# Optimization experiments

Measured on AMD Instinct MI355X. Metric: run time of the kernel, lower is better.

Reference implementation:

```python
import jax, jax.numpy as jnp
import numpy as np

N_NODES = 50000
N_EDGES = 500000
D_FEAT = 128
HIDDEN = 128
EPS = 1e-8


def _lin_init(key, fan_in, fan_out):
    return jax.random.normal(key, (fan_in, fan_out), dtype=jnp.float32) / np.sqrt(fan_in)


def setup_inputs() -> dict:
    key = jax.random.key(0)
    ks = jax.random.split(key, 16)
    h = jax.random.normal(ks[0], (N_NODES, D_FEAT), dtype=jnp.float32)
    coord = jax.random.normal(ks[1], (N_NODES, 3), dtype=jnp.float32)
    vel = jax.random.normal(ks[2], (N_NODES, 3), dtype=jnp.float32)
    edge_index = jax.random.randint(ks[3], (2, N_EDGES), 0, N_NODES, dtype=jnp.int32)
    return {
        "h": h, "coord": coord, "vel": vel, "edge_index": edge_index,
        "W_e1": _lin_init(ks[4], 2 * D_FEAT + 1, HIDDEN), "b_e1": jnp.zeros((HIDDEN,), jnp.float32),
        "W_e2": _lin_init(ks[5], HIDDEN, D_FEAT), "b_e2": jnp.zeros((D_FEAT,), jnp.float32),
        "W_c1": _lin_init(ks[6], D_FEAT, HIDDEN), "b_c1": jnp.zeros((HIDDEN,), jnp.float32),
        "W_c2": _lin_init(ks[7], HIDDEN, 1), "b_c2": jnp.zeros((1,), jnp.float32),
        "W_v1": _lin_init(ks[8], D_FEAT, HIDDEN), "b_v1": jnp.zeros((HIDDEN,), jnp.float32),
        "W_v2": _lin_init(ks[9], HIDDEN, 1), "b_v2": jnp.zeros((1,), jnp.float32),
        "W_n1": _lin_init(ks[10], 2 * D_FEAT, HIDDEN), "b_n1": jnp.zeros((HIDDEN,), jnp.float32),
        "W_n2": _lin_init(ks[11], HIDDEN, D_FEAT), "b_n2": jnp.zeros((D_FEAT,), jnp.float32),
    }


def reference(h, coord, vel, edge_index,
              W_e1, b_e1, W_e2, b_e2,
              W_c1, b_c1, W_c2, b_c2,
              W_v1, b_v1, W_v2, b_v2,
              W_n1, b_n1, W_n2, b_n2):
    act = jax.nn.silu
    r, c = edge_index[0], edge_index[1]
    n = coord.shape[0]

    # coord2radial with normalize=True
    diff = coord[r] - coord[c]                      # [E, 3]
    rad = jnp.sum(diff * diff, axis=-1, keepdims=True)  # [E, 1]
    norm = jnp.sqrt(jax.lax.stop_gradient(rad)) + EPS
    diff = diff / norm

    # edge_op: Linear -> act -> Linear -> act
    edge_in = jnp.concatenate([h[r], h[c], rad], axis=1)  # [E, 2D+1]
    m_ij = act(act(edge_in @ W_e1 + b_e1) @ W_e2 + b_e2)  # [E, D]

    # coord_op: Linear -> act -> Linear (scalar weight per edge)
    weights = act(m_ij @ W_c1 + b_c1) @ W_c2 + b_c2       # [E, 1]
    coors_sum = jax.ops.segment_sum(diff * weights, r, num_segments=n)  # [N, 3]

    # vel_op: Linear -> act -> Linear (scalar per node)
    vel_weights = act(h @ W_v1 + b_v1) @ W_v2 + b_v2      # [N, 1]
    coord_out = coord + coors_sum + vel * vel_weights

    # node aggregation + node_op: Linear -> act -> Linear
    m_i = jax.ops.segment_sum(m_ij, r, num_segments=h.shape[0])  # [N, D]
    agg = jnp.concatenate([h, m_i], axis=1)               # [N, 2D]
    h_out = act(agg @ W_n1 + b_n1) @ W_n2 + b_n2          # [N, D]
    return (h_out, coord_out)
```

## Files before the change

kernel.cpp:

```cpp
#include <hip/hip_runtime.h>
#include <stdint.h>

#define NN 50000
#define NE 500000
#define BLK 256
#define NEB ((NE + 127) / 128)
#define SST 136

#define BARRIER() asm volatile("s_waitcnt lgkmcnt(0)\n\ts_barrier" ::: "memory")

typedef __attribute__((ext_vector_type(8))) short bf16x8;
typedef __attribute__((ext_vector_type(4))) float f32x4;

__device__ __forceinline__ float silu(float x) {
    float e = __expf(-x);
    return x * __builtin_amdgcn_rcpf(1.0f + e);
}
__device__ __forceinline__ float bf2f(unsigned short s) {
    union { unsigned int u; float f; } v; v.u = ((unsigned int)s) << 16; return v.f;
}
__device__ __forceinline__ unsigned short f2bf(float f) {
    union { float f; unsigned int u; } v; v.f = f;
    return (unsigned short)((v.u + 0x7fffu + ((v.u >> 16) & 1u)) >> 16);
}
__device__ __forceinline__ unsigned int pack2(float a, float b) {
    unsigned int r;
    asm("v_cvt_pk_bf16_f32 %0, %1, %2" : "=v"(r) : "v"(a), "v"(b));
    return r;
}
__device__ __forceinline__ bf16x8 packf8(const float* p) {
    float4 f0 = *(const float4*)p; float4 f1 = *(const float4*)(p + 4);
    union { bf16x8 v; unsigned int u[4]; } o;
    o.u[0] = pack2(f0.x, f0.y); o.u[1] = pack2(f0.z, f0.w);
    o.u[2] = pack2(f1.x, f1.y); o.u[3] = pack2(f1.z, f1.w);
    return o.v;
}

__global__ void prep_h(const float* __restrict__ h, unsigned short* __restrict__ hb) {
    int i = blockIdx.x * 256 + threadIdx.x;
    if (i < NN * 128 / 4) {
        float4 v = ((const float4*)h)[i];
        uint2 o; o.x = pack2(v.x, v.y); o.y = pack2(v.z, v.w);
        ((uint2*)hb)[i] = o;
    }
}

__global__ void prep_w(const float* __restrict__ We1, const float* __restrict__ We2,
                       const float* __restrict__ Wc1, const float* __restrict__ Wv1,
                       const float* __restrict__ Wn1, const float* __restrict__ Wn2,
                       unsigned short* __restrict__ Wt1, unsigned short* __restrict__ Wt2,
                       unsigned short* __restrict__ Wt3, unsigned short* __restrict__ Wv1t,
                       unsigned short* __restrict__ Wn1t, unsigned short* __restrict__ Wn2t) {
    int i = blockIdx.x * 256 + threadIdx.x;
    if (i < 32768) {
        int j = i >> 8, k = i & 255;
        Wt1[i] = f2bf(We1[k * 128 + j]);
    } else if (i < 49152) {
        int t = i - 32768; int j = t >> 7, ks = t & 127;
        int k0 = (ks & 7) * 16 + (ks >> 3);
        Wt2[t] = f2bf(We2[k0 * 128 + j]);
    } else if (i < 65536) {
        int t = i - 49152; int j = t >> 7, ks = t & 127;
        int k0 = (ks & 7) * 16 + (ks >> 3);
        Wt3[t] = f2bf(Wc1[k0 * 128 + j]);
    } else if (i < 81920) {
        int t = i - 65536; int j = t >> 7, k = t & 127;
        Wv1t[t] = f2bf(Wv1[k * 128 + j]);
    } else if (i < 114688) {
        int t = i - 81920; int j = t >> 8, k = t & 255;
        int ksrc;
        if (k < 128) ksrc = k;
        else { int ks = k - 128; ksrc = 128 + (ks & 7) * 16 + (ks >> 3); }
// ... 15 lines not shown
    int t = threadIdx.x, idx = blockIdx.x * 256 + t;
    s[t] = (idx < NN) ? deg[idx] : 0;
    __syncthreads();
    for (int off = 128; off > 0; off >>= 1) {
        if (t < off) s[t] += s[t + off];
        __syncthreads();
    }
    if (t == 0) bsum[blockIdx.x] = s[0];
}

__global__ void scan_b(int* __restrict__ bsum) {
    __shared__ int s[256];
    int t = threadIdx.x;
    int v = (t < 196) ? bsum[t] : 0;
    s[t] = v;
    __syncthreads();
    for (int off = 1; off < 256; off <<= 1) {
        int x = (t >= off) ? s[t - off] : 0;
        __syncthreads();
        s[t] += x;
        __syncthreads();
    }
    if (t < 196) bsum[t] = s[t] - v;
}

__global__ void scan_c(const int* __restrict__ deg, const int* __restrict__ bsum,
                       int* __restrict__ rowptr) {
    __shared__ int s[256];
    int t = threadIdx.x, idx = blockIdx.x * 256 + t;
    int v = (idx < NN) ? deg[idx] : 0;
    s[t] = v;
    __syncthreads();
    for (int off = 1; off < 256; off <<= 1) {
        int x = (t >= off) ? s[t - off] : 0;
        __syncthreads();
        s[t] += x;
        __syncthreads();
    }
    if (idx < NN) rowptr[idx] = bsum[blockIdx.x] + s[t] - v;
    if (idx == 0) rowptr[NN] = NE;
}

__global__ void csr_fill(const int* __restrict__ eidx, const int* __restrict__ rowptr,
                         int* __restrict__ cursor,
                         int* __restrict__ csr_r, int* __restrict__ csr_c) {
    int e = blockIdx.x * 256 + threadIdx.x;
    if (e < NE) {
        int r = eidx[e], c = eidx[NE + e];
        int slot = rowptr[r] + atomicAdd(&cursor[r], 1);
        csr_r[slot] = r; csr_c[slot] = c;
    }
}

__device__ __forceinline__ void wpref256(const unsigned short* __restrict__ W, int halfk,
                                         uint4 w[8], int tid) {
#pragma unroll
    for (int t = 0; t < 8; ++t) {
        int idx = tid + t * 256; int j = idx >> 4, g = idx & 15;
        w[t] = *(const uint4*)(W + (size_t)j * 256 + halfk * 128 + g * 8);
    }
}
__device__ __forceinline__ void wpref128(const unsigned short* __restrict__ W,
                                         uint4 w[8], int tid) {
#pragma unroll
    for (int t = 0; t < 8; ++t) {
        int idx = tid + t * 256; int j = idx >> 4, g = idx & 15;
        w[t] = *(const uint4*)(W + (size_t)j * 128 + g * 8);
    }
}
__device__ __forceinline__ void wwrite(const uint4 w[8], unsigned short* sW, int tid) {
#pragma unroll
    for (int t = 0; t < 8; ++t) {
        int idx = tid + t * 256; int j = idx >> 4, g = idx & 15;
        *(uint4*)(sW + j * SST + g * 8) = w[t];
    }
}
__device__ __forceinline__ void mfma4(const bf16x8 a[2][4], const unsigned short* sW,
                                      int l16, int q, f32x4 acc[2][8]) {
#pragma unroll
    for (int kc = 0; kc < 4; ++kc)
#pragma unroll
        for (int ct = 0; ct < 8; ++ct) {
            bf16x8 b = *(const bf16x8*)(sW + (ct * 16 + l16) * SST + kc * 32 + q * 8);
            acc[0][ct] = __builtin_amdgcn_mfma_f32_16x16x32_bf16(a[0][kc], b, acc[0][ct], 0, 0, 0);
            acc[1][ct] = __builtin_amdgcn_mfma_f32_16x16x32_bf16(a[1][kc], b, acc[1][ct], 0, 0, 0);
        }
}

__global__ __launch_bounds__(BLK, 2) void egcl_edge(
    const float* __restrict__ coord,
    const int* __restrict__ csr_r, const int* __restrict__ csr_c,
    const unsigned short* __restrict__ hb,
    const unsigned short* __restrict__ Wt1,
    const unsigned short* __restrict__ Wt2,
    const unsigned short* __restrict__ Wt3,
    const float* __restrict__ We1,
    const float* __restrict__ be1, const float* __restrict__ be2,
    const float* __restrict__ bc1,
    const float* __restrict__ Wc2, const float* __restrict__ bc2,
    float* __restrict__ m_acc, float* __restrict__ c_sum)
{
    __shared__ __align__(16) unsigned short sAb[128 * SST];
    __shared__ __align__(16) unsigned short sW[128 * SST];
    __shared__ float sRad[128], sDif[128][3];
    __shared__ int sSeg[128];
    __shared__ float sBe1[128], sBe2[128], sBc1[128], sWlast[128], sWc2f[128];

    const int tid = threadIdx.x;
    const int wv = tid >> 6, lane = tid & 63, q = lane >> 4, l16 = lane & 15;
    const int e0 = blockIdx.x * 128;

    int nr[2], nc[2];
#pragma unroll
    for (int si = 0; si < 2; ++si) {
        int e = e0 + (wv * 2 + si) * 16 + l16;
        if (e >= NE) e = NE - 1;
        nr[si] = csr_r[e]; nc[si] = csr_c[e];
    }

    if (tid < 128) {
        sBe1[tid] = be1[tid]; sBe2[tid] = be2[tid]; sBc1[tid] = bc1[tid];
        sWlast[tid] = We1[256 * 128 + tid]; sWc2f[tid] = Wc2[tid];
        int s = e0 + tid; int sc = (s < NE) ? s : (NE - 1);
        int r = csr_r[sc], c = csr_c[sc];
        sSeg[tid] = (s < NE) ? r : -1;
        float dx = coord[r * 3 + 0] - coord[c * 3 + 0];
        float dy = coord[r * 3 + 1] - coord[c * 3 + 1];
        float dz = coord[r * 3 + 2] - coord[c * 3 + 2];
        float rad = fmaf(dx, dx, fmaf(dy, dy, dz * dz));
        float inv = 1.0f / (sqrtf(rad) + 1e-8f);
        sRad[tid] = rad;
        sDif[tid][0] = dx * inv; sDif[tid][1] = dy * inv; sDif[tid][2] = dz * inv;
    }

    uint4 wA[8], wB[8];
    wpref256(Wt1, 0, wA, tid);
    wpref256(Wt1, 1, wB, tid);
    bf16x8 ar[2][4], ac[2][4];
#pragma unroll
    for (int si = 0; si < 2; ++si)
#pragma unroll
        for (int kc = 0; kc < 4; ++kc) {
            ar[si][kc] = *(const bf16x8*)(hb + (size_t)nr[si] * 128 + kc * 32 + q * 8);
            ac[si][kc] = *(const bf16x8*)(hb + (size_t)nc[si] * 128 + kc * 32 + q * 8);
        }
    wwrite(wA, sW, tid);
    wwrite(wB, sAb, tid);
    wpref128(Wt2, wA, tid);
    const float bc2v = bc2[0];
    BARRIER();

    f32x4 acc[2][8];
#pragma unroll
    for (int si = 0; si < 2; ++si)
#pragma unroll
        for (int ct = 0; ct < 8; ++ct) acc[si][ct] = (f32x4){0.f, 0.f, 0.f, 0.f};

    mfma4(ar, sW, l16, q, acc);
    mfma4(ac, sAb, l16, q, acc);
    BARRIER();
    wwrite(wA, sW, tid);
    wpref128(Wt3, wA, tid);

#pragma unroll
    for (int si = 0; si < 2; ++si)
#pragma unroll
        for (int r = 0; r < 4; ++r) {
            int row = (wv * 2 + si) * 16 + q * 4 + r;
            float rad = sRad[row];
            float v[8];
#pragma unroll
            for (int ct = 0; ct < 8; ++ct) {
                int col = ct * 16 + l16;
                v[ct] = silu(acc[si][ct][r] + rad * sWlast[col] + sBe1[col]);
            }
            uint4 pk = make_uint4(pack2(v[0], v[1]), pack2(v[2], v[3]),
                                  pack2(v[4], v[5]), pack2(v[6], v[7]));
            *(uint4*)(sAb + row * SST + l16 * 8) = pk;
        }
    BARRIER();

#pragma unroll
    for (int si = 0; si < 2; ++si)
#pragma unroll
        for (int ct = 0; ct < 8; ++ct) acc[si][ct] = (f32x4){0.f, 0.f, 0.f, 0.f};
    {
        bf16x8 a[2][4];
#pragma unroll
        for (int si = 0; si < 2; ++si) {
            int row = (wv * 2 + si) * 16 + l16;
#pragma unroll
            for (int kc = 0; kc < 4; ++kc)
                a[si][kc] = *(const bf16x8*)(sAb + row * SST + kc * 32 + q * 8);
        }
        mfma4(a, sW, l16, q, acc);
    }
#pragma unroll
    for (int si = 0; si < 2; ++si)
#pragma unroll
        for (int r = 0; r < 4; ++r) {
            float v[8];
#pragma unroll
            for (int ct = 0; ct < 8; ++ct) v[ct] = silu(acc[si][ct][r] + sBe2[ct * 16 + l16]);
            int row = (wv * 2 + si) * 16 + q * 4 + r;
            *(uint4*)(sAb + row * SST + l16 * 8) =
                make_uint4(pack2(v[0], v[1]), pack2(v[2], v[3]),
                           pack2(v[4], v[5]), pack2(v[6], v[7]));
        }
    BARRIER();
    wwrite(wA, sW, tid);
    BARRIER();

#pragma unroll
    for (int si = 0; si < 2; ++si)
#pragma unroll
        for (int ct = 0; ct < 8; ++ct) acc[si][ct] = (f32x4){0.f, 0.f, 0.f, 0.f};
    {
        bf16x8 a[2][4];
#pragma unroll
        for (int si = 0; si < 2; ++si) {
            int row = (wv * 2 + si) * 16 + l16;
#pragma unroll
            for (int kc = 0; kc < 4; ++kc)
                a[si][kc] = *(const bf16x8*)(sAb + row * SST + kc * 32 + q * 8);
        }
        mfma4(a, sW, l16, q, acc);
    }
#pragma unroll
    for (int si = 0; si < 2; ++si) {
        float p[4];
#pragma unroll
        for (int r = 0; r < 4; ++r) {
            float s = 0.f;
#pragma unroll
            for (int ct = 0; ct < 8; ++ct) {
                int col = ct * 16 + l16;
                float t = silu(acc[si][ct][r] + sBc1[col]);
                s = fmaf(t, sWc2f[col], s);
            }
            p[r] = s;
        }
#pragma unroll
        for (int m = 1; m < 16; m <<= 1)
#pragma unroll
            for (int r = 0; r < 4; ++r) p[r] += __shfl_xor(p[r], m, 16);
        if (l16 == 0) {
#pragma unroll
            for (int r = 0; r < 4; ++r) {
                int row = (wv * 2 + si) * 16 + q * 4 + r;
                int rn = sSeg[row];
                if (rn >= 0) {
                    float wgt = p[r] + bc2v;
                    atomicAdd(&c_sum[(size_t)rn * 3 + 0], sDif[row][0] * wgt);
                    atomicAdd(&c_sum[(size_t)rn * 3 + 1], sDif[row][1] * wgt);
                    atomicAdd(&c_sum[(size_t)rn * 3 + 2], sDif[row][2] * wgt);
                }
            }
        }
    }

    {
        int p = tid & 127, half = tid >> 7;
        int base = half * 64;
        float run = 0.f;
        int cur = sSeg[base];
        bool openL = true;
#pragma unroll 1
        for (int i0 = 0; i0 < 64; i0 += 4) {
            float v[4]; int rr[4];
#pragma unroll
            for (int j = 0; j < 4; ++j) {
                int row = base + i0 + j;
                rr[j] = sSeg[row];
                v[j] = bf2f(sAb[row * SST + p]);
            }
#pragma unroll
            for (int j = 0; j < 4; ++j) {
                if (rr[j] != cur) {
                    if (cur >= 0) {
                        float* dst = &m_acc[(size_t)cur * 128 + p];
                        if (openL) atomicAdd(dst, run);
                        else       *dst = run;
                    }
                    run = 0.f; cur = rr[j]; openL = false;
                }
                run += v[j];
            }
        }
        if (cur >= 0) atomicAdd(&m_acc[(size_t)cur * 128 + p], run);
    }
}

__global__ __launch_bounds__(BLK, 3) void egcl_node(
    const unsigned short* __restrict__ hb,
    const float* __restrict__ coord,
    const float* __restrict__ vel,
    const unsigned short* __restrict__ Wv1t, const float* __restrict__ bv1,
    const float* __restrict__ Wv2, const float* __restrict__ bv2,
    const unsigned short* __restrict__ Wn1t, const float* __restrict__ bn1,
    const unsigned short* __restrict__ Wn2t, const float* __restrict__ bn2,
    const float* __restrict__ m_acc, const float* __restrict__ c_sum,
    float* __restrict__ out_h, float* __restrict__ out_c)
{
    __shared__ __align__(16) unsigned short sAb[128 * SST];
    __shared__ float sBv1[128], sWv2f[128], sBn1[128], sBn2[128];

    const int tid = threadIdx.x;
    const int wv = tid >> 6, lane = tid & 63, q = lane >> 4, l16 = lane & 15;
    const int n0 = blockIdx.x * 128;
    int nval = NN - n0; if (nval > 128) nval = 128;

    if (tid < 128) {
        sBv1[tid] = bv1[tid]; sWv2f[tid] = Wv2[tid];
        sBn1[tid] = bn1[tid]; sBn2[tid] = bn2[tid];
    }
    const float bv2v = bv2[0];

    bf16x8 ah[2][4], am[2][4];
#pragma unroll
    for (int si = 0; si < 2; ++si) {
        int row = (wv * 2 + si) * 16 + l16;
        int nn = n0 + row; if (nn >= NN) nn = NN - 1;
#pragma unroll
        for (int kc = 0; kc < 4; ++kc) {
            ah[si][kc] = *(const bf16x8*)(hb + (size_t)nn * 128 + kc * 32 + q * 8);
            am[si][kc] = packf8(m_acc + (size_t)nn * 128 + kc * 32 + q * 8);
        }
    }

    BARRIER();

    f32x4 acc[2][8];
#pragma unroll
    for (int si = 0; si < 2; ++si)
#pragma unroll
        for (int ct = 0; ct < 8; ++ct) acc[si][ct] = (f32x4){0.f, 0.f, 0.f, 0.f};
#pragma unroll
    for (int kc = 0; kc < 4; ++kc)
#pragma unroll
        for (int ct = 0; ct < 8; ++ct) {
            bf16x8 b = *(const bf16x8*)(Wv1t + (size_t)(ct * 16 + l16) * 128 + kc * 32 + q * 8);
            acc[0][ct] = __builtin_amdgcn_mfma_f32_16x16x32_bf16(ah[0][kc], b, acc[0][ct], 0, 0, 0);
            acc[1][ct] = __builtin_amdgcn_mfma_f32_16x16x32_bf16(ah[1][kc], b, acc[1][ct], 0, 0, 0);
        }
#pragma unroll
    for (int si = 0; si < 2; ++si) {
// ... 86 lines not shown
    for (int si = 0; si < 2; ++si)
#pragma unroll
        for (int r = 0; r < 4; ++r) {
            int row = (wv * 2 + si) * 16 + q * 4 + r;
            if (row < nval) {
                float* orow = out_h + (size_t)(n0 + row) * 128;
#pragma unroll
                for (int ct = 0; ct < 8; ++ct)
                    orow[ct * 16 + l16] = acc[si][ct][r] + sBn2[ct * 16 + l16];
            }
        }
}

extern "C" void kernel_launch(void* const* d_in, const int* in_sizes, int n_in,
                              void* d_out, int out_size, void* d_ws, size_t ws_size,
                              hipStream_t stream) {
    const float* h     = (const float*)d_in[0];
    const float* coord = (const float*)d_in[1];
    const float* vel   = (const float*)d_in[2];
    const int*   eidx  = (const int*)d_in[3];
    const float* We1 = (const float*)d_in[4];
    const float* be1 = (const float*)d_in[5];
    const float* We2 = (const float*)d_in[6];
    const float* be2 = (const float*)d_in[7];
    const float* Wc1 = (const float*)d_in[8];
    const float* bc1 = (const float*)d_in[9];
    const float* Wc2 = (const float*)d_in[10];
    const float* bc2 = (const float*)d_in[11];
    const float* Wv1 = (const float*)d_in[12];
    const float* bv1 = (const float*)d_in[13];
    const float* Wv2 = (const float*)d_in[14];
    const float* bv2 = (const float*)d_in[15];
    const float* Wn1 = (const float*)d_in[16];
    const float* bn1 = (const float*)d_in[17];
    const float* Wn2 = (const float*)d_in[18];
    const float* bn2 = (const float*)d_in[19];

    char* ws = (char*)d_ws;
    float* m_acc = (float*)ws;
    float* c_sum = (float*)(ws + 25600000);
    unsigned short* hb   = (unsigned short*)(ws + 26200064);
    unsigned short* Wt1  = (unsigned short*)(ws + 39000064);
    unsigned short* Wt2  = (unsigned short*)(ws + 39065600);
    unsigned short* Wt3  = (unsigned short*)(ws + 39098368);
    unsigned short* Wv1t = (unsigned short*)(ws + 39131136);
    unsigned short* Wn1t = (unsigned short*)(ws + 39163904);
    unsigned short* Wn2t = (unsigned short*)(ws + 39229440);
    int* deg    = (int*)(ws + 39262208);
    int* cursor = (int*)(ws + 39462208);
    int* rowptr = (int*)(ws + 39662208);
    int* bsum   = (int*)(ws + 39862272);
    int* csr_r  = (int*)(ws + 39863296);
    int* csr_c  = (int*)(ws + 41863296);

    hipMemsetAsync(ws, 0, 26200000, stream);
    hipMemsetAsync(ws + 39262208, 0, 400000, stream);

    prep_h<<<6250, 256, 0, stream>>>(h, hb);
    prep_w<<<512, 256, 0, stream>>>(We1, We2, Wc1, Wv1, Wn1, Wn2,
                                    Wt1, Wt2, Wt3, Wv1t, Wn1t, Wn2t);

    csr_count<<<1954, 256, 0, stream>>>(eidx, deg);
    scan_a<<<196, 256, 0, stream>>>(deg, bsum);
    scan_b<<<1, 256, 0, stream>>>(bsum);
    scan_c<<<196, 256, 0, stream>>>(deg, bsum, rowptr);
    csr_fill<<<1954, 256, 0, stream>>>(eidx, rowptr, cursor, csr_r, csr_c);

    egcl_edge<<<NEB, BLK, 0, stream>>>(
        coord, csr_r, csr_c, hb, Wt1, Wt2, Wt3,
        We1, be1, be2, bc1, Wc2, bc2, m_acc, c_sum);

    float* out_h = (float*)d_out;
    float* out_c = out_h + (size_t)NN * 128;
    egcl_node<<<(NN + 127) / 128, BLK, 0, stream>>>(
        hb, coord, vel, Wv1t, bv1, Wv2, bv2, Wn1t, bn1, Wn2t, bn2,
        m_acc, c_sum, out_h, out_c);
}
```

Measured before the change: 393.6 us.

## Split edge-kernel work across 8 waves with one 16-row tile each

```diff
diff --git a/kernel.cpp b/kernel.cpp
--- a/kernel.cpp
+++ b/kernel.cpp
@@ -3,7 +3,7 @@
 
 #define NN 50000
 #define NE 500000
-#define BLK 256
+#define EBLK 512
 #define NEB ((NE + 127) / 128)
 #define SST 136
 
@@ -140,41 +140,40 @@
 }
 
 __device__ __forceinline__ void wpref256(const unsigned short* __restrict__ W, int halfk,
-                                         uint4 w[8], int tid) {
-#pragma unroll
-    for (int t = 0; t < 8; ++t) {
-        int idx = tid + t * 256; int j = idx >> 4, g = idx & 15;
+                                         uint4 w[4], int tid) {
+#pragma unroll
+    for (int t = 0; t < 4; ++t) {
+        int idx = tid + t * 512; int j = idx >> 4, g = idx & 15;
         w[t] = *(const uint4*)(W + (size_t)j * 256 + halfk * 128 + g * 8);
     }
 }
 __device__ __forceinline__ void wpref128(const unsigned short* __restrict__ W,
-                                         uint4 w[8], int tid) {
-#pragma unroll
-    for (int t = 0; t < 8; ++t) {
-        int idx = tid + t * 256; int j = idx >> 4, g = idx & 15;
+                                         uint4 w[4], int tid) {
+#pragma unroll
+    for (int t = 0; t < 4; ++t) {
+        int idx = tid + t * 512; int j = idx >> 4, g = idx & 15;
         w[t] = *(const uint4*)(W + (size_t)j * 128 + g * 8);
     }
 }
-__device__ __forceinline__ void wwrite(const uint4 w[8], unsigned short* sW, int tid) {
-#pragma unroll
-    for (int t = 0; t < 8; ++t) {
-        int idx = tid + t * 256; int j = idx >> 4, g = idx & 15;
+__device__ __forceinline__ void wwrite(const uint4 w[4], unsigned short* sW, int tid) {
+#pragma unroll
+    for (int t = 0; t < 4; ++t) {
+        int idx = tid + t * 512; int j = idx >> 4, g = idx & 15;
         *(uint4*)(sW + j * SST + g * 8) = w[t];
     }
 }
-__device__ __forceinline__ void mfma4(const bf16x8 a[2][4], const unsigned short* sW,
-                                      int l16, int q, f32x4 acc[2][8]) {
+__device__ __forceinline__ void mfma4(const bf16x8 a[4], const unsigned short* sW,
+                                      int l16, int q, f32x4 acc[8]) {
 #pragma unroll
     for (int kc = 0; kc < 4; ++kc)
 #pragma unroll
         for (int ct = 0; ct < 8; ++ct) {
             bf16x8 b = *(const bf16x8*)(sW + (ct * 16 + l16) * SST + kc * 32 + q * 8);
-            acc[0][ct] = __builtin_amdgcn_mfma_f32_16x16x32_bf16(a[0][kc], b, acc[0][ct], 0, 0, 0);
-            acc[1][ct] = __builtin_amdgcn_mfma_f32_16x16x32_bf16(a[1][kc], b, acc[1][ct], 0, 0, 0);
-        }
-}
-
-__global__ __launch_bounds__(BLK, 2) void egcl_edge(
+            acc[ct] = __builtin_amdgcn_mfma_f32_16x16x32_bf16(a[kc], b, acc[ct], 0, 0, 0);
+        }
+}
+
+__global__ __launch_bounds__(EBLK, 4) void egcl_edge(
     const float* __restrict__ coord,
     const int* __restrict__ csr_r, const int* __restrict__ csr_c,
     const unsigned short* __restrict__ hb,
@@ -197,13 +196,9 @@
     const int wv = tid >> 6, lane = tid & 63, q = lane >> 4, l16 = lane & 15;
     const int e0 = blockIdx.x * 128;
 
-    int nr[2], nc[2];
-#pragma unroll
-    for (int si = 0; si < 2; ++si) {
-        int e = e0 + (wv * 2 + si) * 16 + l16;
-        if (e >= NE) e = NE - 1;
-        nr[si] = csr_r[e]; nc[si] = csr_c[e];
-    }
+    int er = e0 + wv * 16 + l16;
+    if (er >= NE) er = NE - 1;
+    const int nr = csr_r[er], nc = csr_c[er];
 
     if (tid < 128) {
         sBe1[tid] = be1[tid]; sBe2[tid] = be2[tid]; sBc1[tid] = bc1[tid];
@@ -220,28 +215,24 @@
         sDif[tid][0] = dx * inv; sDif[tid][1] = dy * inv; sDif[tid][2] = dz * inv;
     }
 
-    uint4 wA[8], wB[8];
+    uint4 wA[4], wB[4];
     wpref256(Wt1, 0, wA, tid);
     wpref256(Wt1, 1, wB, tid);
-    bf16x8 ar[2][4], ac[2][4];
-#pragma unroll
-    for (int si = 0; si < 2; ++si)
-#pragma unroll
-        for (int kc = 0; kc < 4; ++kc) {
-            ar[si][kc] = *(const bf16x8*)(hb + (size_t)nr[si] * 128 + kc * 32 + q * 8);
-            ac[si][kc] = *(const bf16x8*)(hb + (size_t)nc[si] * 128 + kc * 32 + q * 8);
-        }
+    bf16x8 ar[4], ac[4];
+#pragma unroll
+    for (int kc = 0; kc < 4; ++kc) {
+        ar[kc] = *(const bf16x8*)(hb + (size_t)nr * 128 + kc * 32 + q * 8);
+        ac[kc] = *(const bf16x8*)(hb + (size_t)nc * 128 + kc * 32 + q * 8);
+    }
     wwrite(wA, sW, tid);
     wwrite(wB, sAb, tid);
     wpref128(Wt2, wA, tid);
     const float bc2v = bc2[0];
     BARRIER();
 
-    f32x4 acc[2][8];
-#pragma unroll
-    for (int si = 0; si < 2; ++si)
-#pragma unroll
-        for (int ct = 0; ct < 8; ++ct) acc[si][ct] = (f32x4){0.f, 0.f, 0.f, 0.f};
+    f32x4 acc[8];
+#pragma unroll
+    for (int ct = 0; ct < 8; ++ct) acc[ct] = (f32x4){0.f, 0.f, 0.f, 0.f};
 
     mfma4(ar, sW, l16, q, acc);
     mfma4(ac, sAb, l16, q, acc);
@@ -250,79 +241,64 @@
     wpref128(Wt3, wA, tid);
 
 #pragma unroll
-    for (int si = 0; si < 2; ++si)
+    for (int r = 0; r < 4; ++r) {
+        int row = wv * 16 + q * 4 + r;
+        float rad = sRad[row];
+        float v[8];
+#pragma unroll
+        for (int ct = 0; ct < 8; ++ct) {
+            int col = ct * 16 + l16;
+            v[ct] = silu(acc[ct][r] + rad * sWlast[col] + sBe1[col]);
+        }
+        uint4 pk = make_uint4(pack2(v[0], v[1]), pack2(v[2], v[3]),
+                              pack2(v[4], v[5]), pack2(v[6], v[7]));
+        *(uint4*)(sAb + row * SST + l16 * 8) = pk;
+    }
+    BARRIER();
+
+#pragma unroll
+    for (int ct = 0; ct < 8; ++ct) acc[ct] = (f32x4){0.f, 0.f, 0.f, 0.f};
+    {
+        bf16x8 a[4];
+        int row = wv * 16 + l16;
+#pragma unroll
+        for (int kc = 0; kc < 4; ++kc)
+            a[kc] = *(const bf16x8*)(sAb + row * SST + kc * 32 + q * 8);
+        mfma4(a, sW, l16, q, acc);
+    }
+#pragma unroll
+    for (int r = 0; r < 4; ++r) {
+        float v[8];
+#pragma unroll
+        for (int ct = 0; ct < 8; ++ct) v[ct] = silu(acc[ct][r] + sBe2[ct * 16 + l16]);
+        int row = wv * 16 + q * 4 + r;
+        *(uint4*)(sAb + row * SST + l16 * 8) =
+            make_uint4(pack2(v[0], v[1]), pack2(v[2], v[3]),
+                       pack2(v[4], v[5]), pack2(v[6], v[7]));
+    }
+    BARRIER();
+    wwrite(wA, sW, tid);
+    BARRIER();
+
+#pragma unroll
+    for (int ct = 0; ct < 8; ++ct) acc[ct] = (f32x4){0.f, 0.f, 0.f, 0.f};
+    {
+        bf16x8 a[4];
+        int row = wv * 16 + l16;
+#pragma unroll
+        for (int kc = 0; kc < 4; ++kc)
+            a[kc] = *(const bf16x8*)(sAb + row * SST + kc * 32 + q * 8);
+        mfma4(a, sW, l16, q, acc);
+    }
+    {
+        float p[4];
 #pragma unroll
         for (int r = 0; r < 4; ++r) {
-            int row = (wv * 2 + si) * 16 + q * 4 + r;
-            float rad = sRad[row];
-            float v[8];
+            float s = 0.f;
 #pragma unroll
             for (int ct = 0; ct < 8; ++ct) {
                 int col = ct * 16 + l16;
-                v[ct] = silu(acc[si][ct][r] + rad * sWlast[col] + sBe1[col]);
-            }
-            uint4 pk = make_uint4(pack2(v[0], v[1]), pack2(v[2], v[3]),
-                                  pack2(v[4], v[5]), pack2(v[6], v[7]));
-            *(uint4*)(sAb + row * SST + l16 * 8) = pk;
-        }
-    BARRIER();
-
-#pragma unroll
-    for (int si = 0; si < 2; ++si)
-#pragma unroll
-        for (int ct = 0; ct < 8; ++ct) acc[si][ct] = (f32x4){0.f, 0.f, 0.f, 0.f};
-    {
-        bf16x8 a[2][4];
-#pragma unroll
-        for (int si = 0; si < 2; ++si) {
-            int row = (wv * 2 + si) * 16 + l16;
-#pragma unroll
-            for (int kc = 0; kc < 4; ++kc)
-                a[si][kc] = *(const bf16x8*)(sAb + row * SST + kc * 32 + q * 8);
-        }
-        mfma4(a, sW, l16, q, acc);
-    }
-#pragma unroll
-    for (int si = 0; si < 2; ++si)
-#pragma unroll
-        for (int r = 0; r < 4; ++r) {
-            float v[8];
-#pragma unroll
-            for (int ct = 0; ct < 8; ++ct) v[ct] = silu(acc[si][ct][r] + sBe2[ct * 16 + l16]);
-            int row = (wv * 2 + si) * 16 + q * 4 + r;
-            *(uint4*)(sAb + row * SST + l16 * 8) =
-                make_uint4(pack2(v[0], v[1]), pack2(v[2], v[3]),
-                           pack2(v[4], v[5]), pack2(v[6], v[7]));
-        }
-    BARRIER();
-    wwrite(wA, sW, tid);
-    BARRIER();
-
-#pragma unroll
-    for (int si = 0; si < 2; ++si)
-#pragma unroll
-        for (int ct = 0; ct < 8; ++ct) acc[si][ct] = (f32x4){0.f, 0.f, 0.f, 0.f};
-    {
-        bf16x8 a[2][4];
-#pragma unroll
-        for (int si = 0; si < 2; ++si) {
-            int row = (wv * 2 + si) * 16 + l16;
-#pragma unroll
-            for (int kc = 0; kc < 4; ++kc)
-                a[si][kc] = *(const bf16x8*)(sAb + row * SST + kc * 32 + q * 8);
-        }
-        mfma4(a, sW, l16, q, acc);
-    }
-#pragma unroll
-    for (int si = 0; si < 2; ++si) {
-        float p[4];
-#pragma unroll
-        for (int r = 0; r < 4; ++r) {
-            float s = 0.f;
-#pragma unroll
-            for (int ct = 0; ct < 8; ++ct) {
-                int col = ct * 16 + l16;
-                float t = silu(acc[si][ct][r] + sBc1[col]);
+                float t = silu(acc[ct][r] + sBc1[col]);
                 s = fmaf(t, sWc2f[col], s);
             }
             p[r] = s;
@@ -334,7 +310,7 @@
         if (l16 == 0) {
 #pragma unroll
             for (int r = 0; r < 4; ++r) {
-                int row = (wv * 2 + si) * 16 + q * 4 + r;
+                int row = wv * 16 + q * 4 + r;
                 int rn = sSeg[row];
                 if (rn >= 0) {
                     float wgt = p[r] + bc2v;
@@ -347,13 +323,13 @@
     }
 
     {
-        int p = tid & 127, half = tid >> 7;
-        int base = half * 64;
+        int p = tid & 127, qtr = tid >> 7;
+        int base = qtr * 32;
         float run = 0.f;
         int cur = sSeg[base];
         bool openL = true;
 #pragma unroll 1
-        for (int i0 = 0; i0 < 64; i0 += 4) {
+        for (int i0 = 0; i0 < 32; i0 += 4) {
             float v[4]; int rr[4];
 #pragma unroll
             for (int j = 0; j < 4; ++j) {
@@ -378,7 +354,7 @@
     }
 }
 
-__global__ __launch_bounds__(BLK, 3) void egcl_node(
+__global__ __launch_bounds__(256, 3) void egcl_node(
     const unsigned short* __restrict__ hb,
     const float* __restrict__ coord,
     const float* __restrict__ vel,
@@ -585,13 +561,13 @@
     scan_c<<<196, 256, 0, stream>>>(deg, bsum, rowptr);
     csr_fill<<<1954, 256, 0, stream>>>(eidx, rowptr, cursor, csr_r, csr_c);
 
-    egcl_edge<<<NEB, BLK, 0, stream>>>(
+    egcl_edge<<<NEB, EBLK, 0, stream>>>(
         coord, csr_r, csr_c, hb, Wt1, Wt2, Wt3,
         We1, be1, be2, bc1, Wc2, bc2, m_acc, c_sum);
 
     float* out_h = (float*)d_out;
     float* out_c = out_h + (size_t)NN * 128;
-    egcl_node<<<(NN + 127) / 128, BLK, 0, stream>>>(
+    egcl_node<<<(NN + 127) / 128, 256, 0, stream>>>(
         hb, coord, vel, Wv1t, bv1, Wv2, bv2, Wn1t, bn1, Wn2t, bn2,
         m_acc, c_sum, out_h, out_c);
 }
```

After: 394.3 us. About the same (+0.2%).

## Split edge-MLP columns across 8 waves with 512-thread edge blocks

Applied to the files above, without the earlier changes.

```diff
diff --git a/kernel.cpp b/kernel.cpp
--- a/kernel.cpp
+++ b/kernel.cpp
@@ -3,7 +3,7 @@
 
 #define NN 50000
 #define NE 500000
-#define BLK 256
+#define EBLK 512
 #define NEB ((NE + 127) / 128)
 #define SST 136
 
@@ -140,41 +140,42 @@
 }
 
 __device__ __forceinline__ void wpref256(const unsigned short* __restrict__ W, int halfk,
-                                         uint4 w[8], int tid) {
-#pragma unroll
-    for (int t = 0; t < 8; ++t) {
-        int idx = tid + t * 256; int j = idx >> 4, g = idx & 15;
+                                         uint4 w[4], int tid) {
+#pragma unroll
+    for (int t = 0; t < 4; ++t) {
+        int idx = tid + t * 512; int j = idx >> 4, g = idx & 15;
         w[t] = *(const uint4*)(W + (size_t)j * 256 + halfk * 128 + g * 8);
     }
 }
 __device__ __forceinline__ void wpref128(const unsigned short* __restrict__ W,
-                                         uint4 w[8], int tid) {
-#pragma unroll
-    for (int t = 0; t < 8; ++t) {
-        int idx = tid + t * 256; int j = idx >> 4, g = idx & 15;
+                                         uint4 w[4], int tid) {
+#pragma unroll
+    for (int t = 0; t < 4; ++t) {
+        int idx = tid + t * 512; int j = idx >> 4, g = idx & 15;
         w[t] = *(const uint4*)(W + (size_t)j * 128 + g * 8);
     }
 }
-__device__ __forceinline__ void wwrite(const uint4 w[8], unsigned short* sW, int tid) {
-#pragma unroll
-    for (int t = 0; t < 8; ++t) {
-        int idx = tid + t * 256; int j = idx >> 4, g = idx & 15;
+__device__ __forceinline__ void wwrite(const uint4 w[4], unsigned short* sW, int tid) {
+#pragma unroll
+    for (int t = 0; t < 4; ++t) {
+        int idx = tid + t * 512; int j = idx >> 4, g = idx & 15;
         *(uint4*)(sW + j * SST + g * 8) = w[t];
     }
 }
-__device__ __forceinline__ void mfma4(const bf16x8 a[2][4], const unsigned short* sW,
-                                      int l16, int q, f32x4 acc[2][8]) {
+__device__ __forceinline__ void mfma_h(const bf16x8 a[2][4], const unsigned short* sB,
+                                       int l16, int q, int ch, f32x4 acc[2][4]) {
 #pragma unroll
     for (int kc = 0; kc < 4; ++kc)
 #pragma unroll
-        for (int ct = 0; ct < 8; ++ct) {
-            bf16x8 b = *(const bf16x8*)(sW + (ct * 16 + l16) * SST + kc * 32 + q * 8);
-            acc[0][ct] = __builtin_amdgcn_mfma_f32_16x16x32_bf16(a[0][kc], b, acc[0][ct], 0, 0, 0);
-            acc[1][ct] = __builtin_amdgcn_mfma_f32_16x16x32_bf16(a[1][kc], b, acc[1][ct], 0, 0, 0);
-        }
-}
-
-__global__ __launch_bounds__(BLK, 2) void egcl_edge(
+        for (int c = 0; c < 4; ++c) {
+            int g = ch * 4 + c;
+            bf16x8 b = *(const bf16x8*)(sB + (g * 16 + l16) * SST + kc * 32 + q * 8);
+            acc[0][c] = __builtin_amdgcn_mfma_f32_16x16x32_bf16(a[0][kc], b, acc[0][c], 0, 0, 0);
+            acc[1][c] = __builtin_amdgcn_mfma_f32_16x16x32_bf16(a[1][kc], b, acc[1][c], 0, 0, 0);
+        }
+}
+
+__global__ __launch_bounds__(EBLK, 4) void egcl_edge(
     const float* __restrict__ coord,
     const int* __restrict__ csr_r, const int* __restrict__ csr_c,
     const unsigned short* __restrict__ hb,
@@ -195,12 +196,14 @@
 
     const int tid = threadIdx.x;
     const int wv = tid >> 6, lane = tid & 63, q = lane >> 4, l16 = lane & 15;
+    const int wq = wv & 3, ch = wv >> 2;
+    const int rb = wq * 32;
     const int e0 = blockIdx.x * 128;
 
     int nr[2], nc[2];
 #pragma unroll
     for (int si = 0; si < 2; ++si) {
-        int e = e0 + (wv * 2 + si) * 16 + l16;
+        int e = e0 + rb + si * 16 + l16;
         if (e >= NE) e = NE - 1;
         nr[si] = csr_r[e]; nc[si] = csr_c[e];
     }
@@ -220,7 +223,7 @@
         sDif[tid][0] = dx * inv; sDif[tid][1] = dy * inv; sDif[tid][2] = dz * inv;
     }
 
-    uint4 wA[8], wB[8];
+    uint4 wA[4], wB[4];
     wpref256(Wt1, 0, wA, tid);
     wpref256(Wt1, 1, wB, tid);
     bf16x8 ar[2][4], ac[2][4];
@@ -237,14 +240,14 @@
     const float bc2v = bc2[0];
     BARRIER();
 
-    f32x4 acc[2][8];
-#pragma unroll
-    for (int si = 0; si < 2; ++si)
-#pragma unroll
-        for (int ct = 0; ct < 8; ++ct) acc[si][ct] = (f32x4){0.f, 0.f, 0.f, 0.f};
-
-    mfma4(ar, sW, l16, q, acc);
-    mfma4(ac, sAb, l16, q, acc);
+    f32x4 acc[2][4];
+#pragma unroll
+    for (int si = 0; si < 2; ++si)
+#pragma unroll
+        for (int c = 0; c < 4; ++c) acc[si][c] = (f32x4){0.f, 0.f, 0.f, 0.f};
+
+    mfma_h(ar, sW, l16, q, ch, acc);
+    mfma_h(ac, sAb, l16, q, ch, acc);
     BARRIER();
     wwrite(wA, sW, tid);
     wpref128(Wt3, wA, tid);
@@ -253,65 +256,70 @@
     for (int si = 0; si < 2; ++si)
 #pragma unroll
         for (int r = 0; r < 4; ++r) {
-            int row = (wv * 2 + si) * 16 + q * 4 + r;
+            int row = rb + si * 16 + q * 4 + r;
             float rad = sRad[row];
-            float v[8];
-#pragma unroll
-            for (int ct = 0; ct < 8; ++ct) {
-                int col = ct * 16 + l16;
-                v[ct] = silu(acc[si][ct][r] + rad * sWlast[col] + sBe1[col]);
-            }
-            uint4 pk = make_uint4(pack2(v[0], v[1]), pack2(v[2], v[3]),
-                                  pack2(v[4], v[5]), pack2(v[6], v[7]));
-            *(uint4*)(sAb + row * SST + l16 * 8) = pk;
+            float v[4];
+#pragma unroll
+            for (int c = 0; c < 4; ++c) {
+                int col = (ch * 4 + c) * 16 + l16;
+                v[c] = silu(acc[si][c][r] + rad * sWlast[col] + sBe1[col]);
+            }
+            *(uint2*)(sAb + row * SST + l16 * 8 + ch * 4) =
+                make_uint2(pack2(v[0], v[1]), pack2(v[2], v[3]));
         }
     BARRIER();
 
 #pragma unroll
     for (int si = 0; si < 2; ++si)
 #pragma unroll
-        for (int ct = 0; ct < 8; ++ct) acc[si][ct] = (f32x4){0.f, 0.f, 0.f, 0.f};
+        for (int c = 0; c < 4; ++c) acc[si][c] = (f32x4){0.f, 0.f, 0.f, 0.f};
     {
         bf16x8 a[2][4];
 #pragma unroll
         for (int si = 0; si < 2; ++si) {
-            int row = (wv * 2 + si) * 16 + l16;
+            int row = rb + si * 16 + l16;
 #pragma unroll
             for (int kc = 0; kc < 4; ++kc)
                 a[si][kc] = *(const bf16x8*)(sAb + row * SST + kc * 32 + q * 8);
         }
-        mfma4(a, sW, l16, q, acc);
-    }
+        mfma_h(a, sW, l16, q, ch, acc);
+    }
+    uint2 mu[2][4];
 #pragma unroll
     for (int si = 0; si < 2; ++si)
 #pragma unroll
         for (int r = 0; r < 4; ++r) {
-            float v[8];
-#pragma unroll
-            for (int ct = 0; ct < 8; ++ct) v[ct] = silu(acc[si][ct][r] + sBe2[ct * 16 + l16]);
-            int row = (wv * 2 + si) * 16 + q * 4 + r;
-            *(uint4*)(sAb + row * SST + l16 * 8) =
-                make_uint4(pack2(v[0], v[1]), pack2(v[2], v[3]),
-                           pack2(v[4], v[5]), pack2(v[6], v[7]));
+            float v[4];
+#pragma unroll
+            for (int c = 0; c < 4; ++c)
+                v[c] = silu(acc[si][c][r] + sBe2[(ch * 4 + c) * 16 + l16]);
+            mu[si][r] = make_uint2(pack2(v[0], v[1]), pack2(v[2], v[3]));
         }
     BARRIER();
+#pragma unroll
+    for (int si = 0; si < 2; ++si)
+#pragma unroll
+        for (int r = 0; r < 4; ++r) {
+            int row = rb + si * 16 + q * 4 + r;
+            *(uint2*)(sAb + row * SST + l16 * 8 + ch * 4) = mu[si][r];
+        }
     wwrite(wA, sW, tid);
     BARRIER();
 
 #pragma unroll
     for (int si = 0; si < 2; ++si)
 #pragma unroll
-        for (int ct = 0; ct < 8; ++ct) acc[si][ct] = (f32x4){0.f, 0.f, 0.f, 0.f};
+        for (int c = 0; c < 4; ++c) acc[si][c] = (f32x4){0.f, 0.f, 0.f, 0.f};
     {
         bf16x8 a[2][4];
 #pragma unroll
         for (int si = 0; si < 2; ++si) {
-            int row = (wv * 2 + si) * 16 + l16;
+            int row = rb + si * 16 + l16;
 #pragma unroll
             for (int kc = 0; kc < 4; ++kc)
                 a[si][kc] = *(const bf16x8*)(sAb + row * SST + kc * 32 + q * 8);
         }
-        mfma4(a, sW, l16, q, acc);
+        mfma_h(a, sW, l16, q, ch, acc);
     }
 #pragma unroll
     for (int si = 0; si < 2; ++si) {
@@ -320,9 +328,9 @@
         for (int r = 0; r < 4; ++r) {
             float s = 0.f;
 #pragma unroll
-            for (int ct = 0; ct < 8; ++ct) {
-                int col = ct * 16 + l16;
-                float t = silu(acc[si][ct][r] + sBc1[col]);
+            for (int c = 0; c < 4; ++c) {
+                int col = (ch * 4 + c) * 16 + l16;
+                float t = silu(acc[si][c][r] + sBc1[col]);
                 s = fmaf(t, sWc2f[col], s);
             }
             p[r] = s;
@@ -334,10 +342,10 @@
         if (l16 == 0) {
 #pragma unroll
             for (int r = 0; r < 4; ++r) {
-                int row = (wv * 2 + si) * 16 + q * 4 + r;
+                int row = rb + si * 16 + q * 4 + r;
                 int rn = sSeg[row];
                 if (rn >= 0) {
-                    float wgt = p[r] + bc2v;
+                    float wgt = p[r] + (ch == 0 ? bc2v : 0.0f);
                     atomicAdd(&c_sum[(size_t)rn * 3 + 0], sDif[row][0] * wgt);
                     atomicAdd(&c_sum[(size_t)rn * 3 + 1], sDif[row][1] * wgt);
                     atomicAdd(&c_sum[(size_t)rn * 3 + 2], sDif[row][2] * wgt);
@@ -347,13 +355,13 @@
     }
 
     {
-        int p = tid & 127, half = tid >> 7;
-        int base = half * 64;
+        int p = tid & 127, qtr = tid >> 7;
+        int base = qtr * 32;
         float run = 0.f;
         int cur = sSeg[base];
         bool openL = true;
 #pragma unroll 1
-        for (int i0 = 0; i0 < 64; i0 += 4) {
+        for (int i0 = 0; i0 < 32; i0 += 4) {
             float v[4]; int rr[4];
 #pragma unroll
             for (int j = 0; j < 4; ++j) {
@@ -378,7 +386,7 @@
     }
 }
 
-__global__ __launch_bounds__(BLK, 3) void egcl_node(
+__global__ __launch_bounds__(256, 3) void egcl_node(
     const unsigned short* __restrict__ hb,
     const float* __restrict__ coord,
     const float* __restrict__ vel,
@@ -585,13 +593,13 @@
     scan_c<<<196, 256, 0, stream>>>(deg, bsum, rowptr);
     csr_fill<<<1954, 256, 0, stream>>>(eidx, rowptr, cursor, csr_r, csr_c);
 
-    egcl_edge<<<NEB, BLK, 0, stream>>>(
+    egcl_edge<<<NEB, EBLK, 0, stream>>>(
         coord, csr_r, csr_c, hb, Wt1, Wt2, Wt3,
         We1, be1, be2, bc1, Wc2, bc2, m_acc, c_sum);
 
     float* out_h = (float*)d_out;
     float* out_c = out_h + (size_t)NN * 128;
-    egcl_node<<<(NN + 127) / 128, BLK, 0, stream>>>(
+    egcl_node<<<(NN + 127) / 128, 256, 0, stream>>>(
         hb, coord, vel, Wv1t, bv1, Wv2, bv2, Wn1t, bn1, Wn2t, bn2,
         m_acc, c_sum, out_h, out_c);
 }
```

New measurement: 447.4 us. +13.7%, slower.

## Precompute per-node first-layer projections and gather them instead of raw features

Applied to the files above, without the earlier changes.

```diff
diff --git a/kernel.cpp b/kernel.cpp
--- a/kernel.cpp
+++ b/kernel.cpp
@@ -3,11 +3,11 @@
 
 #define NN 50000
 #define NE 500000
-#define BLK 256
 #define NEB ((NE + 127) / 128)
 #define SST 136
 
 #define BARRIER() asm volatile("s_waitcnt lgkmcnt(0)\n\ts_barrier" ::: "memory")
+#define WAVE_SYNC() asm volatile("s_waitcnt lgkmcnt(0)" ::: "memory")
 
 typedef __attribute__((ext_vector_type(8))) short bf16x8;
 typedef __attribute__((ext_vector_type(4))) float f32x4;
@@ -18,6 +18,12 @@
 }
 __device__ __forceinline__ float bf2f(unsigned short s) {
     union { unsigned int u; float f; } v; v.u = ((unsigned int)s) << 16; return v.f;
+}
+__device__ __forceinline__ float bflo(unsigned int u) {
+    union { unsigned int u; float f; } v; v.u = u << 16; return v.f;
+}
+__device__ __forceinline__ float bfhi(unsigned int u) {
+    union { unsigned int u; float f; } v; v.u = u & 0xffff0000u; return v.f;
 }
 __device__ __forceinline__ unsigned short f2bf(float f) {
     union { float f; unsigned int u; } v; v.f = f;
@@ -139,27 +145,20 @@
     }
 }
 
-__device__ __forceinline__ void wpref256(const unsigned short* __restrict__ W, int halfk,
-                                         uint4 w[8], int tid) {
+__device__ __forceinline__ void stage256(const unsigned short* __restrict__ W, int halfk,
+                                         unsigned short* sW, int tid) {
 #pragma unroll
     for (int t = 0; t < 8; ++t) {
         int idx = tid + t * 256; int j = idx >> 4, g = idx & 15;
-        w[t] = *(const uint4*)(W + (size_t)j * 256 + halfk * 128 + g * 8);
-    }
-}
-__device__ __forceinline__ void wpref128(const unsigned short* __restrict__ W,
-                                         uint4 w[8], int tid) {
+        *(uint4*)(sW + j * SST + g * 8) = *(const uint4*)(W + (size_t)j * 256 + halfk * 128 + g * 8);
+    }
+}
+__device__ __forceinline__ void stage128(const unsigned short* __restrict__ W,
+                                         unsigned short* sW, int tid) {
 #pragma unroll
     for (int t = 0; t < 8; ++t) {
         int idx = tid + t * 256; int j = idx >> 4, g = idx & 15;
-        w[t] = *(const uint4*)(W + (size_t)j * 128 + g * 8);
-    }
-}
-__device__ __forceinline__ void wwrite(const uint4 w[8], unsigned short* sW, int tid) {
-#pragma unroll
-    for (int t = 0; t < 8; ++t) {
-        int idx = tid + t * 256; int j = idx >> 4, g = idx & 15;
-        *(uint4*)(sW + j * SST + g * 8) = w[t];
+        *(uint4*)(sW + j * SST + g * 8) = *(const uint4*)(W + (size_t)j * 128 + g * 8);
     }
 }
 __device__ __forceinline__ void mfma4(const bf16x8 a[2][4], const unsigned short* sW,
@@ -174,24 +173,84 @@
         }
 }
 
-__global__ __launch_bounds__(BLK, 2) void egcl_edge(
+__global__ __launch_bounds__(256, 2) void prep_P(
+    const unsigned short* __restrict__ hb,
+    const unsigned short* __restrict__ Wt1,
+    unsigned short* __restrict__ P1, unsigned short* __restrict__ P2)
+{
+    __shared__ __align__(16) unsigned short sWa[128 * SST];
+    __shared__ __align__(16) unsigned short sWb[128 * SST];
+    const int tid = threadIdx.x;
+    const int wv = tid >> 6, lane = tid & 63, q = lane >> 4, l16 = lane & 15;
+    const int n0 = blockIdx.x * 128;
+
+    stage256(Wt1, 0, sWa, tid);
+    stage256(Wt1, 1, sWb, tid);
+    bf16x8 ah[2][4];
+#pragma unroll
+    for (int si = 0; si < 2; ++si) {
+        int nn = n0 + (wv * 2 + si) * 16 + l16; if (nn >= NN) nn = NN - 1;
+#pragma unroll
+        for (int kc = 0; kc < 4; ++kc)
+            ah[si][kc] = *(const bf16x8*)(hb + (size_t)nn * 128 + kc * 32 + q * 8);
+    }
+    BARRIER();
+
+    f32x4 acc[2][8];
+#pragma unroll
+    for (int si = 0; si < 2; ++si)
+#pragma unroll
+        for (int ct = 0; ct < 8; ++ct) acc[si][ct] = (f32x4){0.f, 0.f, 0.f, 0.f};
+    mfma4(ah, sWa, l16, q, acc);
+#pragma unroll
+    for (int si = 0; si < 2; ++si)
+#pragma unroll
+        for (int r = 0; r < 4; ++r) {
+            int n = n0 + (wv * 2 + si) * 16 + q * 4 + r;
+            if (n < NN) {
+                uint4 pk = make_uint4(pack2(acc[si][0][r], acc[si][1][r]),
+                                      pack2(acc[si][2][r], acc[si][3][r]),
+                                      pack2(acc[si][4][r], acc[si][5][r]),
+                                      pack2(acc[si][6][r], acc[si][7][r]));
+                *(uint4*)(P1 + (size_t)n * 128 + l16 * 8) = pk;
+            }
+        }
+#pragma unroll
+    for (int si = 0; si < 2; ++si)
+#pragma unroll
+        for (int ct = 0; ct < 8; ++ct) acc[si][ct] = (f32x4){0.f, 0.f, 0.f, 0.f};
+    mfma4(ah, sWb, l16, q, acc);
+#pragma unroll
+    for (int si = 0; si < 2; ++si)
+#pragma unroll
+        for (int r = 0; r < 4; ++r) {
+            int n = n0 + (wv * 2 + si) * 16 + q * 4 + r;
+            if (n < NN) {
+                uint4 pk = make_uint4(pack2(acc[si][0][r], acc[si][1][r]),
+                                      pack2(acc[si][2][r], acc[si][3][r]),
+                                      pack2(acc[si][4][r], acc[si][5][r]),
+                                      pack2(acc[si][6][r], acc[si][7][r]));
+                *(uint4*)(P2 + (size_t)n * 128 + l16 * 8) = pk;
+            }
+        }
+}
+
+__global__ __launch_bounds__(256, 2) void egcl_edge(
     const float* __restrict__ coord,
     const int* __restrict__ csr_r, const int* __restrict__ csr_c,
-    const unsigned short* __restrict__ hb,
-    const unsigned short* __restrict__ Wt1,
-    const unsigned short* __restrict__ Wt2,
-    const unsigned short* __restrict__ Wt3,
+    const unsigned short* __restrict__ P1, const unsigned short* __restrict__ P2,
+    const unsigned short* __restrict__ Wt2, const unsigned short* __restrict__ Wt3,
     const float* __restrict__ We1,
     const float* __restrict__ be1, const float* __restrict__ be2,
     const float* __restrict__ bc1,
     const float* __restrict__ Wc2, const float* __restrict__ bc2,
     float* __restrict__ m_acc, float* __restrict__ c_sum)
 {
-    __shared__ __align__(16) unsigned short sAb[128 * SST];
-    __shared__ __align__(16) unsigned short sW[128 * SST];
+    __shared__ __align__(16) unsigned short sM[128 * SST];
+    __shared__ __align__(16) unsigned short sB3[128 * SST];
     __shared__ float sRad[128], sDif[128][3];
     __shared__ int sSeg[128];
-    __shared__ float sBe1[128], sBe2[128], sBc1[128], sWlast[128], sWc2f[128];
+    __shared__ float sWlS[128], sBe1S[128], sBe2[128], sBc1[128], sWc2f[128];
 
     const int tid = threadIdx.x;
     const int wv = tid >> 6, lane = tid & 63, q = lane >> 4, l16 = lane & 15;
@@ -204,10 +263,19 @@
         if (e >= NE) e = NE - 1;
         nr[si] = csr_r[e]; nc[si] = csr_c[e];
     }
+    bf16x8 pr[2][4], pc[2][4];
+#pragma unroll
+    for (int si = 0; si < 2; ++si)
+#pragma unroll
+        for (int kc = 0; kc < 4; ++kc) {
+            pr[si][kc] = *(const bf16x8*)(P1 + (size_t)nr[si] * 128 + kc * 32 + q * 8);
+            pc[si][kc] = *(const bf16x8*)(P2 + (size_t)nc[si] * 128 + kc * 32 + q * 8);
+        }
 
     if (tid < 128) {
-        sBe1[tid] = be1[tid]; sBe2[tid] = be2[tid]; sBc1[tid] = bc1[tid];
-        sWlast[tid] = We1[256 * 128 + tid]; sWc2f[tid] = Wc2[tid];
+        int k0 = (tid & 7) * 16 + (tid >> 3);
+        sWlS[tid] = We1[256 * 128 + k0]; sBe1S[tid] = be1[k0];
+        sBe2[tid] = be2[tid]; sBc1[tid] = bc1[tid]; sWc2f[tid] = Wc2[tid];
         int s = e0 + tid; int sc = (s < NE) ? s : (NE - 1);
         int r = csr_r[sc], c = csr_c[sc];
         sSeg[tid] = (s < NE) ? r : -1;
@@ -219,99 +287,79 @@
         sRad[tid] = rad;
         sDif[tid][0] = dx * inv; sDif[tid][1] = dy * inv; sDif[tid][2] = dz * inv;
     }
-
-    uint4 wA[8], wB[8];
-    wpref256(Wt1, 0, wA, tid);
-    wpref256(Wt1, 1, wB, tid);
-    bf16x8 ar[2][4], ac[2][4];
-#pragma unroll
-    for (int si = 0; si < 2; ++si)
-#pragma unroll
-        for (int kc = 0; kc < 4; ++kc) {
-            ar[si][kc] = *(const bf16x8*)(hb + (size_t)nr[si] * 128 + kc * 32 + q * 8);
-            ac[si][kc] = *(const bf16x8*)(hb + (size_t)nc[si] * 128 + kc * 32 + q * 8);
-        }
-    wwrite(wA, sW, tid);
-    wwrite(wB, sAb, tid);
-    wpref128(Wt2, wA, tid);
+    stage128(Wt2, sM, tid);
+    stage128(Wt3, sB3, tid);
     const float bc2v = bc2[0];
     BARRIER();
 
+    bf16x8 a[2][4];
+#pragma unroll
+    for (int si = 0; si < 2; ++si) {
+        int row = (wv * 2 + si) * 16 + l16;
+        float rad = sRad[row];
+#pragma unroll
+        for (int kc = 0; kc < 4; ++kc) {
+            const float* wl = sWlS + kc * 32 + q * 8;
+            const float* be = sBe1S + kc * 32 + q * 8;
+            union { bf16x8 v; unsigned int u[4]; } R, C;
+            R.v = pr[si][kc]; C.v = pc[si][kc];
+            float t[8];
+#pragma unroll
+            for (int p = 0; p < 4; ++p) {
+                t[2 * p]     = bflo(R.u[p]) + bflo(C.u[p]);
+                t[2 * p + 1] = bfhi(R.u[p]) + bfhi(C.u[p]);
+            }
+#pragma unroll
+            for (int j = 0; j < 8; ++j)
+                t[j] = silu(fmaf(rad, wl[j], t[j] + be[j]));
+            union { bf16x8 v; unsigned int u[4]; } O;
+            O.u[0] = pack2(t[0], t[1]); O.u[1] = pack2(t[2], t[3]);
+            O.u[2] = pack2(t[4], t[5]); O.u[3] = pack2(t[6], t[7]);
+            a[si][kc] = O.v;
+        }
+    }
+
     f32x4 acc[2][8];
 #pragma unroll
     for (int si = 0; si < 2; ++si)
 #pragma unroll
         for (int ct = 0; ct < 8; ++ct) acc[si][ct] = (f32x4){0.f, 0.f, 0.f, 0.f};
-
-    mfma4(ar, sW, l16, q, acc);
-    mfma4(ac, sAb, l16, q, acc);
+    mfma4(a, sM, l16, q, acc);
+    uint4 mu[2][4];
+#pragma unroll
+    for (int si = 0; si < 2; ++si)
+#pragma unroll
+        for (int r = 0; r < 4; ++r) {
+            float v[8];
+#pragma unroll
+            for (int ct = 0; ct < 8; ++ct) v[ct] = silu(acc[si][ct][r] + sBe2[ct * 16 + l16]);
+            mu[si][r] = make_uint4(pack2(v[0], v[1]), pack2(v[2], v[3]),
+                                   pack2(v[4], v[5]), pack2(v[6], v[7]));
+        }
     BARRIER();
-    wwrite(wA, sW, tid);
-    wpref128(Wt3, wA, tid);
-
 #pragma unroll
     for (int si = 0; si < 2; ++si)
 #pragma unroll
         for (int r = 0; r < 4; ++r) {
             int row = (wv * 2 + si) * 16 + q * 4 + r;
-            float rad = sRad[row];
-            float v[8];
-#pragma unroll
-            for (int ct = 0; ct < 8; ++ct) {
-                int col = ct * 16 + l16;
-                v[ct] = silu(acc[si][ct][r] + rad * sWlast[col] + sBe1[col]);
-            }
-            uint4 pk = make_uint4(pack2(v[0], v[1]), pack2(v[2], v[3]),
-                                  pack2(v[4], v[5]), pack2(v[6], v[7]));
-            *(uint4*)(sAb + row * SST + l16 * 8) = pk;
-        }
-    BARRIER();
+            *(uint4*)(sM + row * SST + l16 * 8) = mu[si][r];
+        }
+    WAVE_SYNC();
 
 #pragma unroll
     for (int si = 0; si < 2; ++si)
 #pragma unroll
         for (int ct = 0; ct < 8; ++ct) acc[si][ct] = (f32x4){0.f, 0.f, 0.f, 0.f};
     {
-        bf16x8 a[2][4];
+        bf16x8 am[2][4];
 #pragma unroll
         for (int si = 0; si < 2; ++si) {
             int row = (wv * 2 + si) * 16 + l16;
 #pragma unroll
             for (int kc = 0; kc < 4; ++kc)
-                a[si][kc] = *(const bf16x8*)(sAb + row * SST + kc * 32 + q * 8);
-        }
-        mfma4(a, sW, l16, q, acc);
-    }
-#pragma unroll
-    for (int si = 0; si < 2; ++si)
-#pragma unroll
-        for (int r = 0; r < 4; ++r) {
-            float v[8];
-#pragma unroll
-            for (int ct = 0; ct < 8; ++ct) v[ct] = silu(acc[si][ct][r] + sBe2[ct * 16 + l16]);
-            int row = (wv * 2 + si) * 16 + q * 4 + r;
-            *(uint4*)(sAb + row * SST + l16 * 8) =
-                make_uint4(pack2(v[0], v[1]), pack2(v[2], v[3]),
-                           pack2(v[4], v[5]), pack2(v[6], v[7]));
-        }
-    BARRIER();
-    wwrite(wA, sW, tid);
-    BARRIER();
-
-#pragma unroll
-    for (int si = 0; si < 2; ++si)
-#pragma unroll
-        for (int ct = 0; ct < 8; ++ct) acc[si][ct] = (f32x4){0.f, 0.f, 0.f, 0.f};
-    {
-        bf16x8 a[2][4];
-#pragma unroll
-        for (int si = 0; si < 2; ++si) {
-            int row = (wv * 2 + si) * 16 + l16;
-#pragma unroll
-            for (int kc = 0; kc < 4; ++kc)
-                a[si][kc] = *(const bf16x8*)(sAb + row * SST + kc * 32 + q * 8);
-        }
-        mfma4(a, sW, l16, q, acc);
+                am[si][kc] = *(const bf16x8*)(sM + row * SST + kc * 32 + q * 8);
+        }
+        mfma4(am, sB3, l16, q, acc);
     }
 #pragma unroll
     for (int si = 0; si < 2; ++si) {
@@ -345,6 +393,7 @@
             }
         }
     }
+    BARRIER();
 
     {
         int p = tid & 127, half = tid >> 7;
@@ -359,7 +408,7 @@
             for (int j = 0; j < 4; ++j) {
                 int row = base + i0 + j;
                 rr[j] = sSeg[row];
-                v[j] = bf2f(sAb[row * SST + p]);
+                v[j] = bf2f(sM[row * SST + p]);
             }
 #pragma unroll
             for (int j = 0; j < 4; ++j) {
@@ -378,7 +427,7 @@
     }
 }
 
-__global__ __launch_bounds__(BLK, 3) void egcl_node(
+__global__ __launch_bounds__(256, 3) void egcl_node(
     const unsigned short* __restrict__ hb,
     const float* __restrict__ coord,
     const float* __restrict__ vel,
@@ -571,6 +620,8 @@
     int* bsum   = (int*)(ws + 39862272);
     int* csr_r  = (int*)(ws + 39863296);
     int* csr_c  = (int*)(ws + 41863296);
+    unsigned short* P1 = (unsigned short*)(ws + 43863296);
+    unsigned short* P2 = (unsigned short*)(ws + 56663296);
 
     hipMemsetAsync(ws, 0, 26200000, stream);
     hipMemsetAsync(ws + 39262208, 0, 400000, stream);
@@ -578,6 +629,7 @@
     prep_h<<<6250, 256, 0, stream>>>(h, hb);
     prep_w<<<512, 256, 0, stream>>>(We1, We2, Wc1, Wv1, Wn1, Wn2,
                                     Wt1, Wt2, Wt3, Wv1t, Wn1t, Wn2t);
+    prep_P<<<(NN + 127) / 128, 256, 0, stream>>>(hb, Wt1, P1, P2);
 
     csr_count<<<1954, 256, 0, stream>>>(eidx, deg);
     scan_a<<<196, 256, 0, stream>>>(deg, bsum);
@@ -585,13 +637,13 @@
     scan_c<<<196, 256, 0, stream>>>(deg, bsum, rowptr);
     csr_fill<<<1954, 256, 0, stream>>>(eidx, rowptr, cursor, csr_r, csr_c);
 
-    egcl_edge<<<NEB, BLK, 0, stream>>>(
-        coord, csr_r, csr_c, hb, Wt1, Wt2, Wt3,
+    egcl_edge<<<NEB, 256, 0, stream>>>(
+        coord, csr_r, csr_c, P1, P2, Wt2, Wt3,
         We1, be1, be2, bc1, Wc2, bc2, m_acc, c_sum);
 
     float* out_h = (float*)d_out;
     float* out_c = out_h + (size_t)NN * 128;
-    egcl_node<<<(NN + 127) / 128, BLK, 0, stream>>>(
+    egcl_node<<<(NN + 127) / 128, 256, 0, stream>>>(
         hb, coord, vel, Wv1t, bv1, Wv2, bv2, Wn1t, bn1, Wn2t, bn2,
         m_acc, c_sum, out_h, out_c);
 }
```

Result: no change. 389.0 us (median of 2 runs) (-1.2%).
